# Performance work log

Measured on AMD Instinct MI355X. Metric: run time of the kernel, lower is better.

Reference implementation:

```python
import jax, jax.numpy as jnp
import numpy as np

FORGET_BIAS = 1.0


def setup_inputs() -> dict:
    key = jax.random.key(0)
    k1, k2, k3, k4 = jax.random.split(key, 4)
    B, T, D, H, C = 512, 128, 256, 256, 128
    x = jax.random.normal(k1, (B, T, D), dtype=jnp.float32)
    # BasicLSTMCell fused kernel: [(D + H), 4*H], gates ordered (i, j, f, o)
    kernel = jax.random.normal(k2, (D + H, 4 * H), dtype=jnp.float32) * 0.05
    bias = jnp.zeros((4 * H,), dtype=jnp.float32)
    w_out = jax.random.normal(k3, (H, C), dtype=jnp.float32) * 0.05
    b_out = jnp.zeros((C,), dtype=jnp.float32)
    return {"x": x, "kernel": kernel, "bias": bias, "w_out": w_out, "b_out": b_out}


def reference(x, kernel, bias, w_out, b_out):
    B, T, D = x.shape
    H = w_out.shape[0]
    x = x.astype(jnp.float32)

    def step(carry, xt):
        c, h = carry
        z = jnp.concatenate([xt, h], axis=-1) @ kernel + bias  # [B, 4H]
        i, j, f, o = jnp.split(z, 4, axis=-1)
        new_c = c * jax.nn.sigmoid(f + FORGET_BIAS) + jax.nn.sigmoid(i) * jnp.tanh(j)
        new_h = jnp.tanh(new_c) * jax.nn.sigmoid(o)
        return (new_c, new_h), new_h

    c0 = jnp.zeros((B, H), dtype=jnp.float32)
    h0 = jnp.zeros((B, H), dtype=jnp.float32)
    xs = jnp.swapaxes(x, 0, 1)  # [T, B, D] -- unstack along time axis 1
    (_, h_last), _ = jax.lax.scan(step, (c0, h0), xs)
    return h_last @ w_out + b_out
```

## Files before the change

kernel.cpp:

```cpp
#include <hip/hip_runtime.h>
#include <hip/hip_fp16.h>
#include <stdint.h>
#include <stddef.h>


typedef __attribute__((ext_vector_type(8))) __bf16 bf16x8;
typedef __attribute__((ext_vector_type(4))) __bf16 bf16x4;
typedef __attribute__((ext_vector_type(4))) float  f32x4;
typedef __attribute__((ext_vector_type(8))) int    i32x8;

#define LDH   264
#define LDF   272
#define ZPS   2097152ull
#define SONE  0x7F7F7F7F
#define LDA   36

__device__ __forceinline__ f32x4 mfma_bf16(bf16x8 a, bf16x8 b, f32x4 c) {
    return __builtin_amdgcn_mfma_f32_16x16x32_bf16(a, b, c, 0, 0, 0);
}
#define EXP2(x) __builtin_amdgcn_exp2f(x)
#define RCP(x)  __builtin_amdgcn_rcpf(x)
#define L2E  1.442695040f
#define L2E2 2.885390082f

__global__ __launch_bounds__(256) void shuffle_w(const float* __restrict__ Wk,
                                                 __bf16* __restrict__ WxF,
                                                 unsigned char* __restrict__ WhF) {
    int id = blockIdx.x * 256 + threadIdx.x;
    if (id < 32768) {
        int lane = id & 63, kt = (id >> 6) & 7, nt = id >> 9;
        int quad = lane >> 4, l16 = lane & 15;
        const float* src = Wk + (size_t)(kt * 32 + quad * 8) * 1024 + nt * 16 + l16;
        __bf16* dst = WxF + ((size_t)(nt * 8 + kt) * 64 + lane) * 8;
#pragma unroll
        for (int j = 0; j < 8; ++j) dst[j] = (__bf16)src[(size_t)j * 1024];
    } else if (id < 40960) {
        int i = id - 32768;
        int lane = i & 63, kt = (i >> 6) & 1, ng = i >> 7;
        int n = ng * 16 + (lane & 15);
        int kb = 256 + kt * 128 + (lane >> 4) * 32;
        int* dst = (int*)(WhF + (((size_t)ng * 2 + kt) * 64 + lane) * 32);
#pragma unroll
        for (int d = 0; d < 8; ++d) {
            float w0 = Wk[(size_t)(kb + 4 * d + 0) * 1024 + n];
            float w1 = Wk[(size_t)(kb + 4 * d + 1) * 1024 + n];
            float w2 = Wk[(size_t)(kb + 4 * d + 2) * 1024 + n];
            float w3 = Wk[(size_t)(kb + 4 * d + 3) * 1024 + n];
            int lo = __builtin_amdgcn_cvt_pk_fp8_f32(w0, w1, 0, false);
            dst[d]  = __builtin_amdgcn_cvt_pk_fp8_f32(w2, w3, lo, true);
        }
    }
}

__global__ __launch_bounds__(256, 2) void xproj(const float* __restrict__ x,
        const __bf16* __restrict__ WxF, const float* __restrict__ bias,
        uint2* __restrict__ Zx) {
    __shared__ __attribute__((aligned(16))) __bf16 As[2][128 * LDA];
    const int tid = threadIdx.x, w = tid >> 6, lane = tid & 63;
    const int l16 = lane & 15, q = lane >> 4;
    const int p = blockIdx.x & 7, bt = blockIdx.x >> 3;
    const int bb = bt & 31, tg = bt >> 5;
    const int wm = w >> 1, wn = w & 1;

    {
#pragma unroll
        for (int i = 0; i < 4; ++i) {
            int s = tid + i * 256, row = s >> 3, f4 = s & 7;
            int b = bb * 16 + (row & 15), t_ = tg * 8 + (row >> 4);
            float4 v = *((const float4*)(x + (size_t)(b * 128 + t_) * 256) + f4);
            bf16x4 c4 = {(__bf16)v.x, (__bf16)v.y, (__bf16)v.z, (__bf16)v.w};
            *(bf16x4*)&As[0][row * LDA + f4 * 4] = c4;
        }
    }
    __syncthreads();

    f32x4 acc[4][4];
#pragma unroll
    for (int tt = 0; tt < 4; ++tt)
#pragma unroll
        for (int nf = 0; nf < 4; ++nf) acc[tt][nf] = (f32x4){0.f, 0.f, 0.f, 0.f};

#pragma unroll
    for (int ks = 0; ks < 8; ++ks) {
        float4 nv[4];
        if (ks < 7) {
#pragma unroll
            for (int i = 0; i < 4; ++i) {
                int s = tid + i * 256, row = s >> 3, f4 = s & 7;
                int b = bb * 16 + (row & 15), t_ = tg * 8 + (row >> 4);
                nv[i] = *((const float4*)(x + (size_t)(b * 128 + t_) * 256 + (size_t)(ks + 1) * 32) + f4);
            }
        }
        bf16x8 wf[4];
#pragma unroll
        for (int nf = 0; nf < 4; ++nf) {
            int ntF = p * 8 + wn * 4 + nf;
            wf[nf] = *(const bf16x8*)&WxF[(((size_t)ntF * 8 + ks) * 64 + lane) * 8];
        }
#pragma unroll
        for (int tt = 0; tt < 4; ++tt) {
            bf16x8 af = *(const bf16x8*)&As[ks & 1][(wm * 64 + tt * 16 + l16) * LDA + q * 8];
#pragma unroll
            for (int nf = 0; nf < 4; ++nf)
                acc[tt][nf] = mfma_bf16(af, wf[nf], acc[tt][nf]);
        }
        if (ks < 7) {
#pragma unroll
            for (int i = 0; i < 4; ++i) {
                int s = tid + i * 256, row = s >> 3, f4 = s & 7;
                bf16x4 c4 = {(__bf16)nv[i].x, (__bf16)nv[i].y, (__bf16)nv[i].z, (__bf16)nv[i].w};
                *(bf16x4*)&As[(ks + 1) & 1][row * LDA + f4 * 4] = c4;
            }
            __syncthreads();
        }
    }

    const float fb = (p == 4 || p == 5) ? 1.0f : 0.0f;
#pragma unroll
    for (int nf = 0; nf < 4; ++nf) {
        int cnt = wn * 4 + nf;
        float bb_ = bias[p * 128 + cnt * 16 + l16] + fb;
#pragma unroll
        for (int tt = 0; tt < 4; ++tt) {
            int t_ = tg * 8 + wm * 4 + tt;
            union { __half h[4]; uint2 u; } pk;
#pragma unroll
            for (int r = 0; r < 4; ++r) pk.h[r] = __float2half(acc[tt][nf][r] + bb_);
            Zx[(size_t)p * ZPS + ((size_t)(bb * 128 + t_) * 8 + cnt) * 64 + q * 16 + l16] = pk.u;
        }
    }
}

#define LSTM_STEP(TT, ZR, ZZU, ZRE, ZZE, RBUF, WBUF)                           \
    {                                                                          \
        i32x8 afr[2];                                                          \
        _Pragma("unroll")                                                      \
        for (int kt = 0; kt < 2; ++kt) {                                       \
            const uint4* ap = (const uint4*)&HtF[RBUF][l16 * LDF + kt * 128 + quad * 32]; \
            uint4 lo = ap[0], hi = ap[1];                                      \
            afr[kt] = (i32x8){(int)lo.x, (int)lo.y, (int)lo.z, (int)lo.w,      \
                              (int)hi.x, (int)hi.y, (int)hi.z, (int)hi.w};     \
        }                                                                      \
        f32x4 acc[8];                                                          \
        _Pragma("unroll")                                                      \
        for (int p = 0; p < 8; ++p) acc[p] = (f32x4){ZZU[p], 0.f, 0.f, 0.f};   \
        {                                                                      \
            int tl = ((TT) + 2 > 127) ? 127 : ((TT) + 2);                      \
            size_t zi = zi0 + (size_t)tl * 512;                                \
            _Pragma("unroll")                                                  \
            for (int p = 0; p < 8; ++p) ZR[p] = Zx[p * ZPS + zi];              \
        }                                                                      \
        __builtin_amdgcn_s_setprio(1);                                         \
        _Pragma("unroll")                                                      \
        for (int kt = 0; kt < 2; ++kt)                                         \
            _Pragma("unroll")                                                  \
            for (int p = 0; p < 8; ++p)                                        \
                acc[p] = __builtin_amdgcn_mfma_scale_f32_16x16x128_f8f6f4(     \
                    afr[kt], wreg[p * 2 + kt], acc[p], 0, 0, 0, SONE, 0, SONE);\
        __builtin_amdgcn_s_setprio(0);                                         \
        _Pragma("unroll")                                                      \
        for (int p = 0; p < 8; ++p) {                                          \
            unsigned w = (quad & 2) ? ZRE[p].y : ZRE[p].x;                     \
            w = (quad & 1) ? (w >> 16) : (w & 0xffff);                         \
            union { unsigned short u; __half h; } cv; cv.u = (unsigned short)w;\
            ZZE[p] = __half2float(cv.h);                                       \
        }                                                                      \
        unsigned char* ldsw = &HtF[WBUF][0];                                   \
        _Pragma("unroll")                                                      \
        for (int hf = 0; hf < 2; ++hf) {                                       \
            float iv = acc[0 + hf][0];                                         \
            float jv = acc[2 + hf][0];                                         \
            float fv = acc[4 + hf][0];                                         \
            float ov = acc[6 + hf][0];                                         \
            float si = RCP(1.f + EXP2(-L2E * iv));                             \
            float sf = RCP(1.f + EXP2(-L2E * fv));                             \
            float so = RCP(1.f + EXP2(-L2E * ov));                             \
            float tj = 2.f * RCP(1.f + EXP2(-L2E2 * jv)) - 1.f;                \
            float c = c_[hf] * sf + si * tj;                                   \
            c_[hf] = c;                                                        \
            float tc = 2.f * RCP(1.f + EXP2(-L2E2 * c)) - 1.f;                 \
            float h = tc * so;                                                 \
            hr[hf] = h;                                                        \
            unsigned pb = (unsigned)__builtin_amdgcn_cvt_pk_fp8_f32(h, h, 0, false); \
            ldsw[(4 * quad) * LDF + hf * 128 + col0] = (unsigned char)pb;      \
        }                                                                      \
        __syncthreads();           \
    }

__global__ __launch_bounds__(512, 2) void lstm_rec(const unsigned char* __restrict__ WhF,
        const uint2* __restrict__ Zx, const float* __restrict__ wout,
        const float* __restrict__ bout, float* __restrict__ out) {
    __shared__ __attribute__((aligned(16))) unsigned char HtF[2][16 * LDF];
    __shared__ __attribute__((aligned(16))) __bf16 HtB[16 * LDH];
    const int tid = threadIdx.x, wv = tid >> 6, lane = tid & 63;
    const int l16 = lane & 15, quad = lane >> 4;
    const int rbblk = blockIdx.x;
    const int rb = rbblk >> 2, qb = rbblk & 3;

    i32x8 wreg[16];
#pragma unroll
    for (int p = 0; p < 8; ++p) {
        int ng = (p >> 1) * 16 + (p & 1) * 8 + wv;
#pragma unroll
        for (int kt = 0; kt < 2; ++kt) {
            const uint4* wp = (const uint4*)(WhF + (((size_t)ng * 2 + kt) * 64 + lane) * 32);
            uint4 lo = wp[0], hi = wp[1];
            wreg[p * 2 + kt] = (i32x8){(int)lo.x, (int)lo.y, (int)lo.z, (int)lo.w,
                                       (int)hi.x, (int)hi.y, (int)hi.z, (int)hi.w};
        }
    }
    for (int i = tid; i < (16 * LDF * 2) / 4; i += 512) ((uint*)HtF[0])[i] = 0u;

    const int col0 = wv * 16 + l16;
    float c_[2] = {0.f, 0.f};
    float hr[2] = {0.f, 0.f};
    const size_t zi0 = ((size_t)rb * 1024 + wv) * 64 + qb * 16 + l16;

    uint2 zrA[8], zrB[8];
    float zzA[8], zzB[8];
#pragma unroll
    for (int p = 0; p < 8; ++p) zrA[p] = Zx[p * ZPS + zi0];
#pragma unroll
    for (int p = 0; p < 8; ++p) zrB[p] = Zx[p * ZPS + zi0 + 512];
#pragma unroll
    for (int p = 0; p < 8; ++p) {
        unsigned w = (quad & 2) ? zrA[p].y : zrA[p].x;
        w = (quad & 1) ? (w >> 16) : (w & 0xffff);
        union { unsigned short u; __half h; } cv; cv.u = (unsigned short)w;
        zzA[p] = __half2float(cv.h);
    }
    __syncthreads();

#pragma unroll 1
    for (int t = 0; t < 128; t += 2) {
        LSTM_STEP(t,     zrA, zzA, zrB, zzB, 0, 1);
        LSTM_STEP(t + 1, zrB, zzB, zrA, zzA, 1, 0);
    }

    for (int i = tid; i < 16 * LDH; i += 512) HtB[i] = (__bf16)0.f;
    __syncthreads();
#pragma unroll
    for (int hf = 0; hf < 2; ++hf)
        HtB[(4 * quad) * LDH + hf * 128 + col0] = (__bf16)hr[hf];
    __syncthreads();

    bf16x8 wo[8];
#pragma unroll
    for (int kt = 0; kt < 8; ++kt) {
        bf16x8 f;
#pragma unroll
        for (int j = 0; j < 8; ++j)
            f[j] = (__bf16)wout[(size_t)(kt * 32 + quad * 8 + j) * 128 + col0];
        wo[kt] = f;
    }
    f32x4 oa = {0.f, 0.f, 0.f, 0.f};
#pragma unroll
    for (int kt = 0; kt < 8; ++kt) {
        bf16x8 af = *(const bf16x8*)&HtB[l16 * LDH + kt * 32 + quad * 8];
        oa = mfma_bf16(af, wo[kt], oa);
    }
    out[(size_t)(rbblk * 4 + quad) * 128 + col0] = oa[0] + bout[col0];
}

extern "C" void kernel_launch(void* const* d_in, const int* in_sizes, int n_in,
                              void* d_out, int out_size, void* d_ws, size_t ws_size,
                              hipStream_t stream) {
    const float* x    = (const float*)d_in[0];
    const float* Wk   = (const float*)d_in[1];
    const float* bias = (const float*)d_in[2];
    const float* wout = (const float*)d_in[3];
    const float* bout = (const float*)d_in[4];
    float* out = (float*)d_out;

    __bf16*        WxF = (__bf16*)d_ws;
    unsigned char* WhF = (unsigned char*)d_ws + 524288;
    uint2*         Zx  = (uint2*)((char*)d_ws + 2097152);

    shuffle_w<<<160, 256, 0, stream>>>(Wk, WxF, WhF);
    xproj<<<4096, 256, 0, stream>>>(x, WxF, bias, Zx);
    lstm_rec<<<128, 512, 0, stream>>>(WhF, Zx, wout, bout, out);
}
```

Measured before the change: 432.6 us.

## Load x tile once per block and loop over all gate panels in xproj

The input projection kernel used to launch one block per (batch tile, time group, gate panel), so each x tile was read from global memory and converted to bf16 eight times. Now each block stages the full 128x256 x tile in LDS once and loops over all eight gate panels, with one eighth as many blocks. This removes the redundant x reads and conversions. In exchange it uses a larger LDS footprint (about 66 KB per block), launches fewer blocks, and drops the software double-buffering of x loads against the MFMAs.

New measurement: 417.3 us. 1.04x faster.

```diff
diff --git a/kernel.cpp b/kernel.cpp
--- a/kernel.cpp
+++ b/kernel.cpp
@@ -13,7 +13,7 @@
 #define LDF   272
 #define ZPS   2097152ull
 #define SONE  0x7F7F7F7F
-#define LDA   36
+#define LDA2  264
 
 __device__ __forceinline__ f32x4 mfma_bf16(bf16x8 a, bf16x8 b, f32x4 c) {
     return __builtin_amdgcn_mfma_f32_16x16x32_bf16(a, b, c, 0, 0, 0);
@@ -55,78 +55,60 @@
 __global__ __launch_bounds__(256, 2) void xproj(const float* __restrict__ x,
         const __bf16* __restrict__ WxF, const float* __restrict__ bias,
         uint2* __restrict__ Zx) {
-    __shared__ __attribute__((aligned(16))) __bf16 As[2][128 * LDA];
+    __shared__ __attribute__((aligned(16))) __bf16 As[128 * LDA2];
     const int tid = threadIdx.x, w = tid >> 6, lane = tid & 63;
     const int l16 = lane & 15, q = lane >> 4;
-    const int p = blockIdx.x & 7, bt = blockIdx.x >> 3;
-    const int bb = bt & 31, tg = bt >> 5;
+    const int bb = blockIdx.x & 31, tg = blockIdx.x >> 5;
     const int wm = w >> 1, wn = w & 1;
 
-    {
-#pragma unroll
-        for (int i = 0; i < 4; ++i) {
-            int s = tid + i * 256, row = s >> 3, f4 = s & 7;
-            int b = bb * 16 + (row & 15), t_ = tg * 8 + (row >> 4);
-            float4 v = *((const float4*)(x + (size_t)(b * 128 + t_) * 256) + f4);
-            bf16x4 c4 = {(__bf16)v.x, (__bf16)v.y, (__bf16)v.z, (__bf16)v.w};
-            *(bf16x4*)&As[0][row * LDA + f4 * 4] = c4;
-        }
-    }
-    __syncthreads();
-
-    f32x4 acc[4][4];
-#pragma unroll
-    for (int tt = 0; tt < 4; ++tt)
-#pragma unroll
-        for (int nf = 0; nf < 4; ++nf) acc[tt][nf] = (f32x4){0.f, 0.f, 0.f, 0.f};
-
-#pragma unroll
-    for (int ks = 0; ks < 8; ++ks) {
-        float4 nv[4];
-        if (ks < 7) {
-#pragma unroll
-            for (int i = 0; i < 4; ++i) {
-                int s = tid + i * 256, row = s >> 3, f4 = s & 7;
-                int b = bb * 16 + (row & 15), t_ = tg * 8 + (row >> 4);
-                nv[i] = *((const float4*)(x + (size_t)(b * 128 + t_) * 256 + (size_t)(ks + 1) * 32) + f4);
+#pragma unroll
+    for (int i = 0; i < 32; ++i) {
+        int s = tid + i * 256, row = s >> 6, f4 = s & 63;
+        int b = bb * 16 + (row & 15), t_ = tg * 8 + (row >> 4);
+        float4 v = *((const float4*)(x + (size_t)(b * 128 + t_) * 256) + f4);
+        bf16x4 c4 = {(__bf16)v.x, (__bf16)v.y, (__bf16)v.z, (__bf16)v.w};
+        *(bf16x4*)&As[row * LDA2 + f4 * 4] = c4;
+    }
+    __syncthreads();
+
+#pragma unroll 1
+    for (int p = 0; p < 8; ++p) {
+        f32x4 acc[4][4];
+#pragma unroll
+        for (int tt = 0; tt < 4; ++tt)
+#pragma unroll
+            for (int nf = 0; nf < 4; ++nf) acc[tt][nf] = (f32x4){0.f, 0.f, 0.f, 0.f};
+
+#pragma unroll
+        for (int ks = 0; ks < 8; ++ks) {
+            bf16x8 wf[4];
+#pragma unroll
+            for (int nf = 0; nf < 4; ++nf) {
+                int ntF = p * 8 + wn * 4 + nf;
+                wf[nf] = *(const bf16x8*)&WxF[(((size_t)ntF * 8 + ks) * 64 + lane) * 8];
             }
-        }
-        bf16x8 wf[4];
+#pragma unroll
+            for (int tt = 0; tt < 4; ++tt) {
+                bf16x8 af = *(const bf16x8*)&As[(wm * 64 + tt * 16 + l16) * LDA2 + ks * 32 + q * 8];
+#pragma unroll
+                for (int nf = 0; nf < 4; ++nf)
+                    acc[tt][nf] = mfma_bf16(af, wf[nf], acc[tt][nf]);
+            }
+        }
+
+        const float fb = (p == 4 || p == 5) ? 1.0f : 0.0f;
 #pragma unroll
         for (int nf = 0; nf < 4; ++nf) {
-            int ntF = p * 8 + wn * 4 + nf;
-            wf[nf] = *(const bf16x8*)&WxF[(((size_t)ntF * 8 + ks) * 64 + lane) * 8];
-        }
-#pragma unroll
-        for (int tt = 0; tt < 4; ++tt) {
-            bf16x8 af = *(const bf16x8*)&As[ks & 1][(wm * 64 + tt * 16 + l16) * LDA + q * 8];
-#pragma unroll
-            for (int nf = 0; nf < 4; ++nf)
-                acc[tt][nf] = mfma_bf16(af, wf[nf], acc[tt][nf]);
-        }
-        if (ks < 7) {
-#pragma unroll
-            for (int i = 0; i < 4; ++i) {
-                int s = tid + i * 256, row = s >> 3, f4 = s & 7;
-                bf16x4 c4 = {(__bf16)nv[i].x, (__bf16)nv[i].y, (__bf16)nv[i].z, (__bf16)nv[i].w};
-                *(bf16x4*)&As[(ks + 1) & 1][row * LDA + f4 * 4] = c4;
+            int cnt = wn * 4 + nf;
+            float bb_ = bias[p * 128 + cnt * 16 + l16] + fb;
+#pragma unroll
+            for (int tt = 0; tt < 4; ++tt) {
+                int t_ = tg * 8 + wm * 4 + tt;
+                union { __half h[4]; uint2 u; } pk;
+#pragma unroll
+                for (int r = 0; r < 4; ++r) pk.h[r] = __float2half(acc[tt][nf][r] + bb_);
+                Zx[(size_t)p * ZPS + ((size_t)(bb * 128 + t_) * 8 + cnt) * 64 + q * 16 + l16] = pk.u;
             }
-            __syncthreads();
-        }
-    }
-
-    const float fb = (p == 4 || p == 5) ? 1.0f : 0.0f;
-#pragma unroll
-    for (int nf = 0; nf < 4; ++nf) {
-        int cnt = wn * 4 + nf;
-        float bb_ = bias[p * 128 + cnt * 16 + l16] + fb;
-#pragma unroll
-        for (int tt = 0; tt < 4; ++tt) {
-            int t_ = tg * 8 + wm * 4 + tt;
-            union { __half h[4]; uint2 u; } pk;
-#pragma unroll
-            for (int r = 0; r < 4; ++r) pk.h[r] = __float2half(acc[tt][nf][r] + bb_);
-            Zx[(size_t)p * ZPS + ((size_t)(bb * 128 + t_) * 8 + cnt) * 64 + q * 16 + l16] = pk.u;
         }
     }
 }
@@ -277,6 +259,6 @@
     uint2*         Zx  = (uint2*)((char*)d_ws + 2097152);
 
     shuffle_w<<<160, 256, 0, stream>>>(Wk, WxF, WhF);
-    xproj<<<4096, 256, 0, stream>>>(x, WxF, bias, Zx);
+    xproj<<<512, 256, 0, stream>>>(x, WxF, bias, Zx);
     lstm_rec<<<128, 512, 0, stream>>>(WhF, Zx, wout, bout, out);
 }
```
